# Optimization experiments

Measured on AMD Instinct MI355X. Metric: run time of the kernel, lower is better.

Reference implementation:

```python
import jax, jax.numpy as jnp
import numpy as np

B, N, M = 1, 16384, 16384
K_NEIGH = 16
KERNEL_SIZE = 15
C_IN, C_OUT = 64, 128
RADIUS = 1.0


def setup_inputs() -> dict:
    key = jax.random.key(0)
    k1, k2, k3, k4, k5 = jax.random.split(key, 5)
    query_points = jax.random.normal(k1, (B, N, 3), dtype=jnp.float32)
    support_points = query_points  # typical KPConv: support == query
    neighbor_idx = jax.random.randint(k2, (B, N, K_NEIGH), 0, M)
    features = jax.random.normal(k3, (B, M, C_IN), dtype=jnp.float32)
    weights = jax.random.normal(k4, (KERNEL_SIZE, C_IN, C_OUT), dtype=jnp.float32) * 0.005
    # kernel points: random unit directions scaled to radius, first fixed at center
    kp = jax.random.normal(k5, (KERNEL_SIZE, 3), dtype=jnp.float32)
    kp = kp / jnp.linalg.norm(kp, axis=1, keepdims=True) * RADIUS
    kernel_points = kp.at[0].set(jnp.zeros(3, dtype=jnp.float32))
    return {
        "query_points": query_points,
        "support_points": support_points,
        "neighbor_idx": neighbor_idx,
        "features": features,
        "weights": weights,
        "kernel_points": kernel_points,
    }


def reference(query_points, support_points, neighbor_idx, features, weights, kernel_points):
    # gather neighbor features and coords: (B,N,k,C), (B,N,k,3)
    gather = jax.vmap(lambda arr, idx: arr[idx])
    neighbor_feats = gather(features, neighbor_idx)
    neighbor_coords = gather(support_points, neighbor_idx)
    # relative coords to query: (B,N,k,3)
    rel = neighbor_coords - query_points[:, :, None, :]
    # distance to each kernel point: (B,N,k,P)
    diff = rel[:, :, :, None, :] - kernel_points[None, None, None, :, :]
    dists = jnp.linalg.norm(diff, axis=-1)
    # linear influence
    infl = jnp.clip(1.0 - dists / RADIUS, 0.0)
    # weighted sum over neighbors -> (B,N,P,C) without materializing (B,N,k,P,C)
    aggregated = jnp.einsum('bnkp,bnkc->bnpc', infl, neighbor_feats)
    # per-kernel-point matmul -> (B,N,C_out)
    return jnp.einsum('bnpc,pco->bno', aggregated, weights)
```

## Files before the change

kernel.cpp:

```cpp
#include <hip/hip_runtime.h>

typedef __attribute__((ext_vector_type(8))) short bf16x8;
typedef __attribute__((ext_vector_type(4))) float f32x4;

constexpr int N_PTS = 16384;
constexpr int KN = 16;
constexpr int P  = 15;
constexpr int CI = 64;
constexpr int CO = 128;
constexpr int QB = 32;
constexpr int KTOT   = P * CI;
constexpr int KSTEPS = KTOT / 32;
constexpr int APITCH = KTOT + 8;
constexpr int PF = 4;
constexpr size_t FB_OFF = 262144;

static __device__ __forceinline__ unsigned short f2bf(float f) {
    unsigned u = __float_as_uint(f);
    u = (u + 0x7fffu + ((u >> 16) & 1u)) >> 16;
    return (unsigned short)u;
}
#define BFLO(u) __uint_as_float((unsigned)(u) << 16)
#define BFHI(u) __uint_as_float((unsigned)(u) & 0xFFFF0000u)

__global__ __launch_bounds__(256) void prep(const float* __restrict__ W,
                                            const float* __restrict__ feats,
                                            unsigned short* __restrict__ WB,
                                            unsigned short* __restrict__ featsB) {
    const int t = blockIdx.x * 256 + threadIdx.x;

    {
        const float4* src = (const float4*)feats;
        #pragma unroll
        for (int i = 0; i < 8; ++i) {
            const int e = i * 32768 + t;
            const float4 v = src[e];
            uint2 o;
            o.x = f2bf(v.x) | ((unsigned)f2bf(v.y) << 16);
            o.y = f2bf(v.z) | ((unsigned)f2bf(v.w) << 16);
            *(uint2*)&featsB[(size_t)e * 4] = o;
        }
    }

    if (t < 15360) {
        const int l  = t & 63;
        const int kb = (t >> 9) * 32 + ((l >> 4) * 8);
        const int o  = ((t >> 6) & 7) * 16 + (l & 15);
        unsigned short v[8];
        #pragma unroll
        for (int j = 0; j < 8; ++j) v[j] = f2bf(W[(size_t)(kb + j) * CO + o]);
        uint4 q;
        q.x = v[0] | ((unsigned)v[1] << 16);
        q.y = v[2] | ((unsigned)v[3] << 16);
        q.z = v[4] | ((unsigned)v[5] << 16);
        q.w = v[6] | ((unsigned)v[7] << 16);
        *(uint4*)&WB[(size_t)t * 8] = q;
    }
}

__global__ __launch_bounds__(512, 4) void kpconv_main(
    const float* __restrict__ query,
    const float* __restrict__ support,
    const int*   __restrict__ nidx,
    const unsigned short* __restrict__ featsB,
    const unsigned short* __restrict__ WB,
    const float* __restrict__ kp,
    float* __restrict__ out)
{
    __shared__ float sKp[P][3];
    __shared__ unsigned short sIdxS[QB][KN];
    __shared__ int sCnt[QB];
    __shared__ unsigned char sKlist[QB][KN];
    __shared__ __align__(16) unsigned short sInflB[QB][KN][16];
    __shared__ __align__(16) unsigned short sAgg[QB][APITCH];

    const int t  = threadIdx.x;
    const int n0 = blockIdx.x * QB;
    const int w  = t >> 6, l = t & 63;

    if (t < P * 3) ((float*)sKp)[t] = kp[t];
    if (t < QB) sCnt[t] = 0;
    __syncthreads();

    {
        const int pt = t >> 4, k = t & 15;
        const int n = n0 + pt;
        const int idx = nidx[n * KN + k];
        sIdxS[pt][k] = (unsigned short)idx;
        const float rx = support[idx * 3 + 0] - query[n * 3 + 0];
        const float ry = support[idx * 3 + 1] - query[n * 3 + 1];
        const float rz = support[idx * 3 + 2] - query[n * 3 + 2];
        unsigned short h[16];
        float mx = 0.0f;
        #pragma unroll
        for (int p = 0; p < P; ++p) {
            const float dx = rx - sKp[p][0];
            const float dy = ry - sKp[p][1];
            const float dz = rz - sKp[p][2];
            const float infl = fmaxf(1.0f - sqrtf(dx*dx + dy*dy + dz*dz), 0.0f);
            mx = fmaxf(mx, infl);
            h[p] = f2bf(infl);
        }
        h[15] = 0;
        uint4 u0, u1;
        u0.x = h[0] | ((unsigned)h[1] << 16);   u0.y = h[2] | ((unsigned)h[3] << 16);
        u0.z = h[4] | ((unsigned)h[5] << 16);   u0.w = h[6] | ((unsigned)h[7] << 16);
        u1.x = h[8] | ((unsigned)h[9] << 16);   u1.y = h[10] | ((unsigned)h[11] << 16);
        u1.z = h[12] | ((unsigned)h[13] << 16); u1.w = h[14];
        *(uint4*)&sInflB[pt][k][0] = u0;
        *(uint4*)&sInflB[pt][k][8] = u1;
        if (mx > 0.0f) {
            const int slot = atomicAdd(&sCnt[pt], 1);
            sKlist[pt][slot] = (unsigned char)k;
        }
    }
    __syncthreads();

    {
        const int pt = t >> 4;
        const int c  = (t & 15) * 4;
        const int nk = sCnt[pt];
        f32x4 A0={0,0,0,0},A1={0,0,0,0},A2={0,0,0,0},A3={0,0,0,0},A4={0,0,0,0};
        f32x4 A5={0,0,0,0},A6={0,0,0,0},A7={0,0,0,0},A8={0,0,0,0},A9={0,0,0,0};
        f32x4 A10={0,0,0,0},A11={0,0,0,0},A12={0,0,0,0},A13={0,0,0,0},A14={0,0,0,0};
        for (int i = 0; i < nk; ++i) {
            const int k   = sKlist[pt][i];
            const int idx = sIdxS[pt][k];
            const uint2 fu = *(const uint2*)&featsB[(size_t)idx * CI + c];
            const f32x4 fv = { BFLO(fu.x), BFHI(fu.x), BFLO(fu.y), BFHI(fu.y) };
            const uint4 u0 = *(const uint4*)&sInflB[pt][k][0];
            const uint4 u1 = *(const uint4*)&sInflB[pt][k][8];
            A0  += BFLO(u0.x) * fv;  A1  += BFHI(u0.x) * fv;
            A2  += BFLO(u0.y) * fv;  A3  += BFHI(u0.y) * fv;
            A4  += BFLO(u0.z) * fv;  A5  += BFHI(u0.z) * fv;
            A6  += BFLO(u0.w) * fv;  A7  += BFHI(u0.w) * fv;
            A8  += BFLO(u1.x) * fv;  A9  += BFHI(u1.x) * fv;
            A10 += BFLO(u1.y) * fv;  A11 += BFHI(u1.y) * fv;
            A12 += BFLO(u1.z) * fv;  A13 += BFHI(u1.z) * fv;
            A14 += BFLO(u1.w) * fv;
        }
        #define STORE_P(p, Ap)                                                  \
            do {                                                                \
                uint2 wv;                                                       \
                wv.x = f2bf(Ap.x) | ((unsigned)f2bf(Ap.y) << 16);               \
                wv.y = f2bf(Ap.z) | ((unsigned)f2bf(Ap.w) << 16);               \
                *(uint2*)&sAgg[pt][(p) * CI + c] = wv;                          \
            } while (0)
        STORE_P(0, A0);  STORE_P(1, A1);  STORE_P(2, A2);  STORE_P(3, A3);
        STORE_P(4, A4);  STORE_P(5, A5);  STORE_P(6, A6);  STORE_P(7, A7);
        STORE_P(8, A8);  STORE_P(9, A9);  STORE_P(10, A10); STORE_P(11, A11);
        STORE_P(12, A12); STORE_P(13, A13); STORE_P(14, A14);
        #undef STORE_P
    }
    __syncthreads();

    {
        f32x4 c0 = {0.f, 0.f, 0.f, 0.f};
        f32x4 c1 = {0.f, 0.f, 0.f, 0.f};
        const int kq = (l >> 4) * 8;
        const unsigned short* a0 = &sAgg[l & 15][kq];
        const unsigned short* a1 = &sAgg[16 + (l & 15)][kq];
        const unsigned short* wb = &WB[(size_t)(w * 64 + l) * 8];
        bf16x8 pb[PF];
        #pragma unroll
        for (int s = 0; s < PF; ++s) pb[s] = *(const bf16x8*)&wb[(size_t)s * 4096];
        #pragma unroll
        for (int s = 0; s < KSTEPS; ++s) {
            const bf16x8 av0 = *(const bf16x8*)&a0[s * 32];
            const bf16x8 av1 = *(const bf16x8*)&a1[s * 32];
            const bf16x8 bv = pb[s & (PF - 1)];
            c0 = __builtin_amdgcn_mfma_f32_16x16x32_bf16(av0, bv, c0, 0, 0, 0);
            c1 = __builtin_amdgcn_mfma_f32_16x16x32_bf16(av1, bv, c1, 0, 0, 0);
            if (s + PF < KSTEPS) pb[s & (PF - 1)] = *(const bf16x8*)&wb[(size_t)(s + PF) * 4096];
        }
        const int o0 = w * 16 + (l & 15);
        const int r0 = n0 + (l >> 4) * 4;
        #pragma unroll
        for (int r = 0; r < 4; ++r) {
            out[(size_t)(r0 + r) * CO + o0]      = c0[r];
            out[(size_t)(r0 + 16 + r) * CO + o0] = c1[r];
        }
    }
}

extern "C" void kernel_launch(void* const* d_in, const int* in_sizes, int n_in,
                              void* d_out, int out_size, void* d_ws, size_t ws_size,
                              hipStream_t stream) {
    const float* query   = (const float*)d_in[0];
    const float* support = (const float*)d_in[1];
    const int*   nidx    = (const int*)d_in[2];
    const float* feats   = (const float*)d_in[3];
    const float* W       = (const float*)d_in[4];
    const float* kp      = (const float*)d_in[5];
    float* out = (float*)d_out;
    unsigned short* WB     = (unsigned short*)d_ws;
    unsigned short* featsB = (unsigned short*)((char*)d_ws + FB_OFF);

    hipLaunchKernelGGL(prep, dim3(128), dim3(256), 0, stream, W, feats, WB, featsB);
    hipLaunchKernelGGL(kpconv_main, dim3(N_PTS / QB), dim3(512), 0, stream,
                       query, support, nidx, featsB, WB, kp, out);
}
```

Measured before the change: 88.36 us.

## Drop neighbor compaction and prefetch feature rows before influence computation

```diff
diff --git a/kernel.cpp b/kernel.cpp
--- a/kernel.cpp
+++ b/kernel.cpp
@@ -41,7 +41,6 @@
             *(uint2*)&featsB[(size_t)e * 4] = o;
         }
     }
-
     if (t < 15360) {
         const int l  = t & 63;
         const int kb = (t >> 9) * 32 + ((l >> 4) * 8);
@@ -69,37 +68,49 @@
 {
     __shared__ float sKp[P][3];
     __shared__ unsigned short sIdxS[QB][KN];
-    __shared__ int sCnt[QB];
-    __shared__ unsigned char sKlist[QB][KN];
     __shared__ __align__(16) unsigned short sInflB[QB][KN][16];
     __shared__ __align__(16) unsigned short sAgg[QB][APITCH];
 
     const int t  = threadIdx.x;
     const int n0 = blockIdx.x * QB;
     const int w  = t >> 6, l = t & 63;
-
+    const int pt = t >> 4, x = t & 15;
+    const int n  = n0 + pt;
+    const int c  = 4 * x;
+
+    const int myIdx = nidx[n * KN + x];
+    sIdxS[pt][x] = (unsigned short)myIdx;
+    const float sx = support[myIdx * 3 + 0];
+    const float sy = support[myIdx * 3 + 1];
+    const float sz = support[myIdx * 3 + 2];
+    const float qx = query[n * 3 + 0];
+    const float qy = query[n * 3 + 1];
+    const float qz = query[n * 3 + 2];
     if (t < P * 3) ((float*)sKp)[t] = kp[t];
-    if (t < QB) sCnt[t] = 0;
     __syncthreads();
 
-    {
-        const int pt = t >> 4, k = t & 15;
-        const int n = n0 + pt;
-        const int idx = nidx[n * KN + k];
-        sIdxS[pt][k] = (unsigned short)idx;
-        const float rx = support[idx * 3 + 0] - query[n * 3 + 0];
-        const float ry = support[idx * 3 + 1] - query[n * 3 + 1];
-        const float rz = support[idx * 3 + 2] - query[n * 3 + 2];
+    const uint4 iv0 = *(const uint4*)&sIdxS[pt][0];
+    const uint4 iv1 = *(const uint4*)&sIdxS[pt][8];
+    #define ROWLD(word, hi) \
+        (*(const uint2*)&featsB[(size_t)((hi) ? ((word) >> 16) : ((word) & 0xFFFFu)) * CI + c])
+    const uint2 f0 = ROWLD(iv0.x, 0);
+    const uint2 f1 = ROWLD(iv0.x, 1);
+    const uint2 f2 = ROWLD(iv0.y, 0);
+    const uint2 f3 = ROWLD(iv0.y, 1);
+    const uint2 f4 = ROWLD(iv0.z, 0);
+    const uint2 f5 = ROWLD(iv0.z, 1);
+    const uint2 f6 = ROWLD(iv0.w, 0);
+    const uint2 f7 = ROWLD(iv0.w, 1);
+
+    {
+        const float rx = sx - qx, ry = sy - qy, rz = sz - qz;
         unsigned short h[16];
-        float mx = 0.0f;
         #pragma unroll
         for (int p = 0; p < P; ++p) {
             const float dx = rx - sKp[p][0];
             const float dy = ry - sKp[p][1];
             const float dz = rz - sKp[p][2];
-            const float infl = fmaxf(1.0f - sqrtf(dx*dx + dy*dy + dz*dz), 0.0f);
-            mx = fmaxf(mx, infl);
-            h[p] = f2bf(infl);
+            h[p] = f2bf(fmaxf(1.0f - sqrtf(dx*dx + dy*dy + dz*dz), 0.0f));
         }
         h[15] = 0;
         uint4 u0, u1;
@@ -107,38 +118,47 @@
         u0.z = h[4] | ((unsigned)h[5] << 16);   u0.w = h[6] | ((unsigned)h[7] << 16);
         u1.x = h[8] | ((unsigned)h[9] << 16);   u1.y = h[10] | ((unsigned)h[11] << 16);
         u1.z = h[12] | ((unsigned)h[13] << 16); u1.w = h[14];
-        *(uint4*)&sInflB[pt][k][0] = u0;
-        *(uint4*)&sInflB[pt][k][8] = u1;
-        if (mx > 0.0f) {
-            const int slot = atomicAdd(&sCnt[pt], 1);
-            sKlist[pt][slot] = (unsigned char)k;
-        }
+        *(uint4*)&sInflB[pt][x][0] = u0;
+        *(uint4*)&sInflB[pt][x][8] = u1;
     }
     __syncthreads();
 
     {
-        const int pt = t >> 4;
-        const int c  = (t & 15) * 4;
-        const int nk = sCnt[pt];
+        const uint2 f8  = ROWLD(iv1.x, 0);
+        const uint2 f9  = ROWLD(iv1.x, 1);
+        const uint2 f10 = ROWLD(iv1.y, 0);
+        const uint2 f11 = ROWLD(iv1.y, 1);
+        const uint2 f12 = ROWLD(iv1.z, 0);
+        const uint2 f13 = ROWLD(iv1.z, 1);
+        const uint2 f14 = ROWLD(iv1.w, 0);
+        const uint2 f15 = ROWLD(iv1.w, 1);
+
         f32x4 A0={0,0,0,0},A1={0,0,0,0},A2={0,0,0,0},A3={0,0,0,0},A4={0,0,0,0};
         f32x4 A5={0,0,0,0},A6={0,0,0,0},A7={0,0,0,0},A8={0,0,0,0},A9={0,0,0,0};
         f32x4 A10={0,0,0,0},A11={0,0,0,0},A12={0,0,0,0},A13={0,0,0,0},A14={0,0,0,0};
-        for (int i = 0; i < nk; ++i) {
-            const int k   = sKlist[pt][i];
-            const int idx = sIdxS[pt][k];
-            const uint2 fu = *(const uint2*)&featsB[(size_t)idx * CI + c];
-            const f32x4 fv = { BFLO(fu.x), BFHI(fu.x), BFLO(fu.y), BFHI(fu.y) };
-            const uint4 u0 = *(const uint4*)&sInflB[pt][k][0];
-            const uint4 u1 = *(const uint4*)&sInflB[pt][k][8];
-            A0  += BFLO(u0.x) * fv;  A1  += BFHI(u0.x) * fv;
-            A2  += BFLO(u0.y) * fv;  A3  += BFHI(u0.y) * fv;
-            A4  += BFLO(u0.z) * fv;  A5  += BFHI(u0.z) * fv;
-            A6  += BFLO(u0.w) * fv;  A7  += BFHI(u0.w) * fv;
-            A8  += BFLO(u1.x) * fv;  A9  += BFHI(u1.x) * fv;
-            A10 += BFLO(u1.y) * fv;  A11 += BFHI(u1.y) * fv;
-            A12 += BFLO(u1.z) * fv;  A13 += BFHI(u1.z) * fv;
-            A14 += BFLO(u1.w) * fv;
-        }
+
+        #define FMA_K(FR, K)                                                    \
+            do {                                                                \
+                const uint4 u0 = *(const uint4*)&sInflB[pt][K][0];              \
+                const uint4 u1 = *(const uint4*)&sInflB[pt][K][8];              \
+                const f32x4 fv = { BFLO(FR.x), BFHI(FR.x),                      \
+                                   BFLO(FR.y), BFHI(FR.y) };                    \
+                A0  += BFLO(u0.x) * fv;  A1  += BFHI(u0.x) * fv;                \
+                A2  += BFLO(u0.y) * fv;  A3  += BFHI(u0.y) * fv;                \
+                A4  += BFLO(u0.z) * fv;  A5  += BFHI(u0.z) * fv;                \
+                A6  += BFLO(u0.w) * fv;  A7  += BFHI(u0.w) * fv;                \
+                A8  += BFLO(u1.x) * fv;  A9  += BFHI(u1.x) * fv;                \
+                A10 += BFLO(u1.y) * fv;  A11 += BFHI(u1.y) * fv;                \
+                A12 += BFLO(u1.z) * fv;  A13 += BFHI(u1.z) * fv;                \
+                A14 += BFLO(u1.w) * fv;                                         \
+            } while (0)
+        FMA_K(f0, 0);   FMA_K(f1, 1);   FMA_K(f2, 2);   FMA_K(f3, 3);
+        FMA_K(f4, 4);   FMA_K(f5, 5);   FMA_K(f6, 6);   FMA_K(f7, 7);
+        FMA_K(f8, 8);   FMA_K(f9, 9);   FMA_K(f10, 10); FMA_K(f11, 11);
+        FMA_K(f12, 12); FMA_K(f13, 13); FMA_K(f14, 14); FMA_K(f15, 15);
+        #undef FMA_K
+        #undef ROWLD
+
         #define STORE_P(p, Ap)                                                  \
             do {                                                                \
                 uint2 wv;                                                       \
```

Result: no change. 88.43 us (+0.1%).
